# Kernel tuning notes

Hardware: AMD Instinct MI355X
Metric: run time of the kernel (lower is better)

The kernel has to match this reference:

```python
import jax, jax.numpy as jnp
import numpy as np

NUM_HEADS = 8

def _proj(x, W, b):
    # 1x1 conv == channel-wise linear: x [B,Ci,H,W], W [Co,Ci], b [Co]
    return jnp.einsum('oi,bihw->bohw', W, x) + b[None, :, None, None]

def setup_inputs() -> dict:
    key = jax.random.key(0)
    ks = jax.random.split(key, 8)
    B, Cin, Cout, H, W = 4, 256, 256, 48, 48
    s = 1.0 / np.sqrt(Cin).astype(np.float32)
    return {
        'queries': jax.random.normal(ks[0], (B, Cin, H, W), jnp.float32),
        'keys':    jax.random.normal(ks[1], (B, Cin, H, W), jnp.float32),
        'values':  jax.random.normal(ks[2], (B, Cin, H, W), jnp.float32),
        'Wq': jax.random.normal(ks[3], (Cout, Cin), jnp.float32) * s,
        'bq': jnp.zeros((Cout,), jnp.float32),
        'Wk': jax.random.normal(ks[4], (Cout, Cin), jnp.float32) * s,
        'bk': jnp.zeros((Cout,), jnp.float32),
        'Wv': jax.random.normal(ks[5], (Cout, Cin), jnp.float32) * s,
        'bv': jnp.zeros((Cout,), jnp.float32),
        'Wo': jax.random.normal(ks[6], (Cout, Cout), jnp.float32) * s,
        'bo': jnp.zeros((Cout,), jnp.float32),
    }

def reference(queries, keys, values, Wq, bq, Wk, bk, Wv, bv, Wo, bo):
    B, _, H, W = values.shape
    Cout = Wq.shape[0]
    d = Cout // NUM_HEADS
    # project and split heads: [B, heads, d, N]
    q = _proj(queries, Wq, bq).reshape(B, NUM_HEADS, d, H * W)
    k = _proj(keys,    Wk, bk).reshape(B, NUM_HEADS, d, H * W)
    v = _proj(values,  Wv, bv).reshape(B, NUM_HEADS, d, H * W)
    scale = 1.0 / np.sqrt(Cout).astype(np.float32)  # source scales by sqrt(out_channels)
    attn = jax.nn.softmax(jnp.einsum('bhdn,bhdm->bhnm', q, k) * scale, axis=-1)
    out = jnp.einsum('bhdm,bhnm->bhdn', v, attn).reshape(B, Cout, H, W)
    return _proj(out, Wo, bo)
```

## Files before the change

kernel.cpp:

```cpp
#include <hip/hip_runtime.h>
#include <hip/hip_bf16.h>

#define NTOT 2304
#define CIN  256
#define DHEAD 32

typedef float  f32x4  __attribute__((ext_vector_type(4)));
typedef __bf16 bf16x8 __attribute__((ext_vector_type(8)));
typedef unsigned short u16x8 __attribute__((ext_vector_type(8)));

static __device__ __forceinline__ unsigned short f2bf(float f) {
    unsigned int u = __float_as_uint(f);
    u += 0x7fff + ((u >> 16) & 1);
    return (unsigned short)(u >> 16);
}

static __device__ __forceinline__ unsigned int pk2(float a, float b) {
    unsigned int r;
    asm("v_cvt_pk_bf16_f32 %0, %1, %2" : "=v"(r) : "v"(a), "v"(b));
    return r;
}

union U8 { unsigned short s[8]; bf16x8 v; };
union PB { unsigned int u[4]; bf16x8 v; };

__global__ __launch_bounds__(256) void pack_weights_kernel(
    const float* __restrict__ Wq, const float* __restrict__ bq,
    const float* __restrict__ Wk, const float* __restrict__ Wv,
    const float* __restrict__ Wo,
    unsigned short* __restrict__ Wq_b, unsigned short* __restrict__ Wk_b,
    unsigned short* __restrict__ Wv_b, unsigned short* __restrict__ Wo_b,
    float* __restrict__ bq_s)
{
    const float SQ = 1.44269504088896340736f / 16.0f;
    int i = blockIdx.x * 256 + threadIdx.x;
    Wq_b[i] = f2bf(Wq[i] * SQ);
    Wk_b[i] = f2bf(Wk[i]);
    Wv_b[i] = f2bf(Wv[i]);
    Wo_b[i] = f2bf(Wo[i]);
    if (blockIdx.x == 0) bq_s[threadIdx.x] = bq[threadIdx.x] * SQ;
}

__global__ __launch_bounds__(256) void proj_all_kernel(
    const float* __restrict__ qx, const float* __restrict__ kx,
    const float* __restrict__ vx,
    const unsigned short* __restrict__ Wqb, const unsigned short* __restrict__ Wkb,
    const unsigned short* __restrict__ Wvb,
    const float* __restrict__ bqs, const float* __restrict__ bk,
    const float* __restrict__ bv,
    unsigned short* __restrict__ Qa, unsigned short* __restrict__ Ka,
    unsigned short* __restrict__ Vp)
{
    const int which = blockIdx.z >> 2;
    const int b     = blockIdx.z & 3;
    const float* x = (which == 0) ? qx : (which == 1) ? kx : vx;
    const unsigned short* Wb = (which == 0) ? Wqb : (which == 1) ? Wkb : Wvb;
    const float* bias = (which == 0) ? bqs : (which == 1) ? bk : bv;
    unsigned short* out = (which == 0) ? Qa : (which == 1) ? Ka : Vp;

    const int n0  = blockIdx.x * 64;
    const int co0 = blockIdx.y * 64;
    const int t = threadIdx.x;
    const int lane = t & 63, w = t >> 6;
    const int g = lane >> 4, l15 = lane & 15;
    const int n_off  = (w & 1) * 32;
    const int co_off = (w >> 1) * 32;

    f32x4 acc[2][2] = {};
    const float* xb = x + (size_t)b * CIN * NTOT;

    for (int ci0 = 0; ci0 < CIN; ci0 += 32) {
        bf16x8 aF[2], bF[2];
        #pragma unroll
        for (int rn = 0; rn < 2; rn++) {
            const float* xp = xb + (size_t)(ci0 + 8 * g) * NTOT + (n0 + n_off + 16 * rn + l15);
            U8 a;
            #pragma unroll
            for (int j = 0; j < 8; j++) a.s[j] = f2bf(xp[(size_t)j * NTOT]);
            aF[rn] = a.v;
        }
        #pragma unroll
        for (int rc = 0; rc < 2; rc++)
            bF[rc] = *reinterpret_cast<const bf16x8*>(
                Wb + (size_t)(co0 + co_off + 16 * rc + l15) * CIN + ci0 + 8 * g);
        #pragma unroll
        for (int rn = 0; rn < 2; rn++)
            #pragma unroll
            for (int rc = 0; rc < 2; rc++)
                acc[rn][rc] = __builtin_amdgcn_mfma_f32_16x16x32_bf16(aF[rn], bF[rc], acc[rn][rc], 0, 0, 0);
    }

    #pragma unroll
    for (int rn = 0; rn < 2; rn++)
    #pragma unroll
    for (int rc = 0; rc < 2; rc++) {
        int co = co0 + co_off + 16 * rc + l15;
        float bs = bias[co];
        int bh = b * 8 + (co >> 5);
        int dd = co & 31;
        int nb = n0 + n_off + 16 * rn + 4 * g;
        if (which == 2) {
            ushort4 v;
            v.x = f2bf(acc[rn][rc][0] + bs);
            v.y = f2bf(acc[rn][rc][1] + bs);
            v.z = f2bf(acc[rn][rc][2] + bs);
            v.w = f2bf(acc[rn][rc][3] + bs);
            int pos = (nb & ~31) + 8 * ((nb >> 2) & 3) + 4 * ((nb >> 4) & 1);
            *reinterpret_cast<ushort4*>(out + ((size_t)bh * DHEAD + dd) * NTOT + pos) = v;
        } else {
            #pragma unroll
            for (int reg = 0; reg < 4; reg++)
                out[((size_t)bh * NTOT + (nb + reg)) * DHEAD + dd] = f2bf(acc[rn][rc][reg] + bs);
        }
    }
}

__global__ __launch_bounds__(256) void attn_kernel(
    const unsigned short* __restrict__ Qa,
    const unsigned short* __restrict__ Ka,
    const unsigned short* __restrict__ Vp,
    unsigned short* __restrict__ Ot)
{
    __shared__ __align__(16) float olds_a[3][64][17];
    __shared__ __align__(16) float olds_b[3][64][17];
    __shared__ float plsum_a[3][64][3];
    __shared__ float plsum_b[3][64][3];
    __shared__ __align__(16) unsigned short tlds[32][40];
    const int f = blockIdx.x;
    const int c = f & 7;
    const int k = f >> 3;
    const int kq = k / 36;
    const int bh = 4 * c + kq;
    const int qt = k - kq * 36;
    const int b = bh >> 3, h = bh & 7;
    const int t = threadIdx.x;
    const int w = t >> 6, lane = t & 63;
    const int g = lane >> 4, l15 = lane & 15;
    const int n_w = qt * 64;
    const int kw0 = w * 576;

    const unsigned short* Kb = Ka + (size_t)bh * NTOT * DHEAD + l15 * DHEAD + 8 * g;
    const unsigned short* V0 = Vp + ((size_t)bh * DHEAD +      l15) * NTOT + 8 * g;
    const unsigned short* V1 = Vp + ((size_t)bh * DHEAD + 16 + l15) * NTOT + 8 * g;

    bf16x8 qBa[2], qBb[2];
    #pragma unroll
    for (int r = 0; r < 2; r++) {
        qBa[r] = *reinterpret_cast<const bf16x8*>(
            Qa + ((size_t)bh * NTOT + n_w + 16 * r + l15) * DHEAD + 8 * g);
        qBb[r] = *reinterpret_cast<const bf16x8*>(
            Qa + ((size_t)bh * NTOT + n_w + 32 + 16 * r + l15) * DHEAD + 8 * g);
    }

    f32x4 oacc_a[2][2] = {};
    f32x4 oacc_b[2][2] = {};
    float psum_a[2] = {0.f, 0.f};
    float psum_b[2] = {0.f, 0.f};
    const f32x4 z4 = {0.f, 0.f, 0.f, 0.f};

    bf16x8 kA[4], kN[4], vA[4], vN[4];
    #pragma unroll
    for (int mc = 0; mc < 4; mc++) {
        kA[mc] = *reinterpret_cast<const bf16x8*>(Kb + (size_t)(kw0 + 16 * mc) * DHEAD);
        kN[mc] = *reinterpret_cast<const bf16x8*>(Kb + (size_t)(kw0 + 64 + 16 * mc) * DHEAD);
    }
    vA[0] = *reinterpret_cast<const bf16x8*>(V0 + kw0);
    vA[1] = *reinterpret_cast<const bf16x8*>(V0 + kw0 + 32);
    vA[2] = *reinterpret_cast<const bf16x8*>(V1 + kw0);
    vA[3] = *reinterpret_cast<const bf16x8*>(V1 + kw0 + 32);
    vN[0] = *reinterpret_cast<const bf16x8*>(V0 + kw0 + 64);
    vN[1] = *reinterpret_cast<const bf16x8*>(V0 + kw0 + 96);
    vN[2] = *reinterpret_cast<const bf16x8*>(V1 + kw0 + 64);
    vN[3] = *reinterpret_cast<const bf16x8*>(V1 + kw0 + 96);

    for (int it = 0; it < 9; it++) {
        {
            f32x4 s[2][4];
            #pragma unroll
            for (int r = 0; r < 2; r++)
                #pragma unroll
                for (int mc = 0; mc < 4; mc++)
                    s[r][mc] = __builtin_amdgcn_mfma_f32_16x16x32_bf16(kA[mc], qBa[r], z4, 0, 0, 0);

            float p[2][4][4];
            #pragma unroll
            for (int r = 0; r < 2; r++) {
                #pragma unroll
                for (int mc = 0; mc < 4; mc++)
                    #pragma unroll
                    for (int reg = 0; reg < 4; reg++)
                        p[r][mc][reg] = __builtin_amdgcn_exp2f(s[r][mc][reg]);
                float t0 = (p[r][0][0] + p[r][0][1]) + (p[r][0][2] + p[r][0][3]);
                float t1 = (p[r][1][0] + p[r][1][1]) + (p[r][1][2] + p[r][1][3]);
                float t2 = (p[r][2][0] + p[r][2][1]) + (p[r][2][2] + p[r][2][3]);
                float t3 = (p[r][3][0] + p[r][3][1]) + (p[r][3][2] + p[r][3][3]);
                psum_a[r] += (t0 + t1) + (t2 + t3);
            }

            PB pb[2][2];
            #pragma unroll
            for (int r = 0; r < 2; r++)
                #pragma unroll
                for (int hh = 0; hh < 2; hh++) {
                    pb[r][hh].u[0] = pk2(p[r][2*hh][0],   p[r][2*hh][1]);
                    pb[r][hh].u[1] = pk2(p[r][2*hh][2],   p[r][2*hh][3]);
                    pb[r][hh].u[2] = pk2(p[r][2*hh+1][0], p[r][2*hh+1][1]);
                    pb[r][hh].u[3] = pk2(p[r][2*hh+1][2], p[r][2*hh+1][3]);
                }

            #pragma unroll
            for (int r = 0; r < 2; r++) {
                oacc_a[r][0] = __builtin_amdgcn_mfma_f32_16x16x32_bf16(vA[0], pb[r][0].v, oacc_a[r][0], 0, 0, 0);
                oacc_a[r][0] = __builtin_amdgcn_mfma_f32_16x16x32_bf16(vA[1], pb[r][1].v, oacc_a[r][0], 0, 0, 0);
                oacc_a[r][1] = __builtin_amdgcn_mfma_f32_16x16x32_bf16(vA[2], pb[r][0].v, oacc_a[r][1], 0, 0, 0);
                oacc_a[r][1] = __builtin_amdgcn_mfma_f32_16x16x32_bf16(vA[3], pb[r][1].v, oacc_a[r][1], 0, 0, 0);
            }
        }
        {
            f32x4 s[2][4];
            #pragma unroll
            for (int r = 0; r < 2; r++)
                #pragma unroll
                for (int mc = 0; mc < 4; mc++)
                    s[r][mc] = __builtin_amdgcn_mfma_f32_16x16x32_bf16(kA[mc], qBb[r], z4, 0, 0, 0);

            float p[2][4][4];
            #pragma unroll
            for (int r = 0; r < 2; r++) {
                #pragma unroll
                for (int mc = 0; mc < 4; mc++)
                    #pragma unroll
                    for (int reg = 0; reg < 4; reg++)
                        p[r][mc][reg] = __builtin_amdgcn_exp2f(s[r][mc][reg]);
                float t0 = (p[r][0][0] + p[r][0][1]) + (p[r][0][2] + p[r][0][3]);
                float t1 = (p[r][1][0] + p[r][1][1]) + (p[r][1][2] + p[r][1][3]);
                float t2 = (p[r][2][0] + p[r][2][1]) + (p[r][2][2] + p[r][2][3]);
                float t3 = (p[r][3][0] + p[r][3][1]) + (p[r][3][2] + p[r][3][3]);
                psum_b[r] += (t0 + t1) + (t2 + t3);
            }

            PB pb[2][2];
            #pragma unroll
            for (int r = 0; r < 2; r++)
                #pragma unroll
                for (int hh = 0; hh < 2; hh++) {
                    pb[r][hh].u[0] = pk2(p[r][2*hh][0],   p[r][2*hh][1]);
                    pb[r][hh].u[1] = pk2(p[r][2*hh][2],   p[r][2*hh][3]);
                    pb[r][hh].u[2] = pk2(p[r][2*hh+1][0], p[r][2*hh+1][1]);
                    pb[r][hh].u[3] = pk2(p[r][2*hh+1][2], p[r][2*hh+1][3]);
                }

            #pragma unroll
            for (int r = 0; r < 2; r++) {
                oacc_b[r][0] = __builtin_amdgcn_mfma_f32_16x16x32_bf16(vA[0], pb[r][0].v, oacc_b[r][0], 0, 0, 0);
                oacc_b[r][0] = __builtin_amdgcn_mfma_f32_16x16x32_bf16(vA[1], pb[r][1].v, oacc_b[r][0], 0, 0, 0);
                oacc_b[r][1] = __builtin_amdgcn_mfma_f32_16x16x32_bf16(vA[2], pb[r][0].v, oacc_b[r][1], 0, 0, 0);
                oacc_b[r][1] = __builtin_amdgcn_mfma_f32_16x16x32_bf16(vA[3], pb[r][1].v, oacc_b[r][1], 0, 0, 0);
            }
        }

        int m2 = kw0 + (it + 2) * 64;
        if (it >= 7) m2 = kw0;
        #pragma unroll
        for (int mc = 0; mc < 4; mc++) {
            kA[mc] = kN[mc];
            kN[mc] = *reinterpret_cast<const bf16x8*>(Kb + (size_t)(m2 + 16 * mc) * DHEAD);
        }
        vA[0] = vN[0]; vA[1] = vN[1]; vA[2] = vN[2]; vA[3] = vN[3];
        vN[0] = *reinterpret_cast<const bf16x8*>(V0 + m2);
        vN[1] = *reinterpret_cast<const bf16x8*>(V0 + m2 + 32);
        vN[2] = *reinterpret_cast<const bf16x8*>(V1 + m2);
        vN[3] = *reinterpret_cast<const bf16x8*>(V1 + m2 + 32);
    }

    if (w > 0) {
        #pragma unroll
        for (int r = 0; r < 2; r++)
            #pragma unroll
            for (int dc = 0; dc < 2; dc++) {
                *reinterpret_cast<f32x4*>(&olds_a[w - 1][lane][8 * r + 4 * dc]) = oacc_a[r][dc];
                *reinterpret_cast<f32x4*>(&olds_b[w - 1][lane][8 * r + 4 * dc]) = oacc_b[r][dc];
            }
        plsum_a[w - 1][lane][0] = psum_a[0];
        plsum_a[w - 1][lane][1] = psum_a[1];
        plsum_b[w - 1][lane][0] = psum_b[0];
        plsum_b[w - 1][lane][1] = psum_b[1];
    }
    __syncthreads();
    if (w == 0) {
        #pragma unroll
        for (int ww = 0; ww < 3; ww++) {
            #pragma unroll
            for (int r = 0; r < 2; r++)
                #pragma unroll
                for (int dc = 0; dc < 2; dc++)
                    oacc_a[r][dc] += *reinterpret_cast<const f32x4*>(&olds_a[ww][lane][8 * r + 4 * dc]);
            psum_a[0] += plsum_a[ww][lane][0];
            psum_a[1] += plsum_a[ww][lane][1];
        }
        float lra[2];
        #pragma unroll
        for (int r = 0; r < 2; r++) {
            float ps = psum_a[r];
            ps += __shfl_xor(ps, 16);
            ps += __shfl_xor(ps, 32);
            lra[r] = 1.0f / ps;
        }
        #pragma unroll
        for (int r = 0; r < 2; r++)
            #pragma unroll
            for (int dc = 0; dc < 2; dc++) {
                ushort4 v;
                v.x = f2bf(oacc_a[r][dc][0] * lra[r]);
                v.y = f2bf(oacc_a[r][dc][1] * lra[r]);
                v.z = f2bf(oacc_a[r][dc][2] * lra[r]);
                v.w = f2bf(oacc_a[r][dc][3] * lra[r]);
                *reinterpret_cast<ushort4*>(&tlds[16 * r + l15][16 * dc + 4 * g]) = v;
            }
        #pragma unroll
        for (int i = 0; i < 2; i++) {
            int row = 16 * i + (lane >> 2), seg = lane & 3;
            u16x8 val = *reinterpret_cast<const u16x8*>(&tlds[row][seg * 8]);
            *reinterpret_cast<u16x8*>(
                Ot + ((size_t)b * NTOT + n_w + row) * CIN + h * DHEAD + seg * 8) = val;
        }

        #pragma unroll
        for (int ww = 0; ww < 3; ww++) {
            #pragma unroll
            for (int r = 0; r < 2; r++)
                #pragma unroll
                for (int dc = 0; dc < 2; dc++)
                    oacc_b[r][dc] += *reinterpret_cast<const f32x4*>(&olds_b[ww][lane][8 * r + 4 * dc]);
            psum_b[0] += plsum_b[ww][lane][0];
            psum_b[1] += plsum_b[ww][lane][1];
        }
        float lrb[2];
        #pragma unroll
        for (int r = 0; r < 2; r++) {
            float ps = psum_b[r];
            ps += __shfl_xor(ps, 16);
            ps += __shfl_xor(ps, 32);
            lrb[r] = 1.0f / ps;
        }
        #pragma unroll
        for (int r = 0; r < 2; r++)
            #pragma unroll
            for (int dc = 0; dc < 2; dc++) {
                ushort4 v;
                v.x = f2bf(oacc_b[r][dc][0] * lrb[r]);
                v.y = f2bf(oacc_b[r][dc][1] * lrb[r]);
                v.z = f2bf(oacc_b[r][dc][2] * lrb[r]);
                v.w = f2bf(oacc_b[r][dc][3] * lrb[r]);
                *reinterpret_cast<ushort4*>(&tlds[16 * r + l15][16 * dc + 4 * g]) = v;
            }
        #pragma unroll
        for (int i = 0; i < 2; i++) {
            int row = 16 * i + (lane >> 2), seg = lane & 3;
            u16x8 val = *reinterpret_cast<const u16x8*>(&tlds[row][seg * 8]);
            *reinterpret_cast<u16x8*>(
                Ot + ((size_t)b * NTOT + n_w + 32 + row) * CIN + h * DHEAD + seg * 8) = val;
        }
    }
}

__global__ __launch_bounds__(256) void out_proj_kernel(
    const unsigned short* __restrict__ Ot,
    const unsigned short* __restrict__ Wob,
    const float* __restrict__ bo,
    float* __restrict__ out)
{
    const int b   = blockIdx.z;
    const int n0  = blockIdx.x * 64;
    const int co0 = blockIdx.y * 64;
    const int t = threadIdx.x;
    const int lane = t & 63, w = t >> 6;
    const int g = lane >> 4, l15 = lane & 15;
    const int n_off  = (w & 1) * 32;
    const int co_off = (w >> 1) * 32;

    f32x4 acc[2][2] = {};
    for (int ci0 = 0; ci0 < CIN; ci0 += 32) {
        bf16x8 aF[2], bF[2];
        #pragma unroll
        for (int rn = 0; rn < 2; rn++)
            aF[rn] = *reinterpret_cast<const bf16x8*>(
                Ot + ((size_t)b * NTOT + n0 + n_off + 16 * rn + l15) * CIN + ci0 + 8 * g);
        #pragma unroll
        for (int rc = 0; rc < 2; rc++)
            bF[rc] = *reinterpret_cast<const bf16x8*>(
                Wob + (size_t)(co0 + co_off + 16 * rc + l15) * CIN + ci0 + 8 * g);
        #pragma unroll
        for (int rn = 0; rn < 2; rn++)
            #pragma unroll
            for (int rc = 0; rc < 2; rc++)
                acc[rn][rc] = __builtin_amdgcn_mfma_f32_16x16x32_bf16(aF[rn], bF[rc], acc[rn][rc], 0, 0, 0);
    }

    #pragma unroll
    for (int rn = 0; rn < 2; rn++)
    #pragma unroll
    for (int rc = 0; rc < 2; rc++) {
        int co = co0 + co_off + 16 * rc + l15;
        float bias = bo[co];
        int nb = n0 + n_off + 16 * rn + 4 * g;
        float4 v;
        v.x = acc[rn][rc][0] + bias;
        v.y = acc[rn][rc][1] + bias;
        v.z = acc[rn][rc][2] + bias;
        v.w = acc[rn][rc][3] + bias;
        *reinterpret_cast<float4*>(out + ((size_t)b * CIN + co) * NTOT + nb) = v;
    }
}

extern "C" void kernel_launch(void* const* d_in, const int* in_sizes, int n_in,
                              void* d_out, int out_size, void* d_ws, size_t ws_size,
                              hipStream_t stream) {
    const float* qx = (const float*)d_in[0];
    const float* kx = (const float*)d_in[1];
    const float* vx = (const float*)d_in[2];
    const float* Wq = (const float*)d_in[3];
    const float* bq = (const float*)d_in[4];
    const float* Wk = (const float*)d_in[5];
    const float* bk = (const float*)d_in[6];
    const float* Wv = (const float*)d_in[7];
    const float* bv = (const float*)d_in[8];
    const float* Wo = (const float*)d_in[9];
    const float* bo = (const float*)d_in[10];
    float* out = (float*)d_out;

    char* ws = (char*)d_ws;
    unsigned short* Wq_b = (unsigned short*)(ws + 0);
    unsigned short* Wk_b = (unsigned short*)(ws + 131072);
    unsigned short* Wv_b = (unsigned short*)(ws + 262144);
    unsigned short* Wo_b = (unsigned short*)(ws + 393216);
    float*          bq_s = (float*)(ws + 524288);
    unsigned short* Qa   = (unsigned short*)(ws + 525312);
    unsigned short* Ka   = (unsigned short*)(ws + 525312 + 1 * 4718592);
    unsigned short* Vp   = (unsigned short*)(ws + 525312 + 2 * 4718592);
    unsigned short* Ot   = (unsigned short*)(ws + 525312 + 3 * 4718592);

    pack_weights_kernel<<<256, 256, 0, stream>>>(Wq, bq, Wk, Wv, Wo,
                                                 Wq_b, Wk_b, Wv_b, Wo_b, bq_s);
    proj_all_kernel<<<dim3(36, 4, 12), 256, 0, stream>>>(
        qx, kx, vx, Wq_b, Wk_b, Wv_b, bq_s, bk, bv, Qa, Ka, Vp);
    attn_kernel<<<dim3(1152), 256, 0, stream>>>(Qa, Ka, Vp, Ot);
    out_proj_kernel<<<dim3(36, 4, 4), 256, 0, stream>>>(Ot, Wo_b, bo, out);
}
```

Baseline: 94.92 us.

## Compute all output channels per projection block to read activations once

The QKV projection kernel now has each block cover all 256 output channels for its 64 spatial positions. Each wave handles 16 positions across 16 channel tiles, where before it handled a 32x32 sub-tile. The fp32 activations are loaded and converted to bf16 once instead of four times, at the cost of 64 accumulator registers per lane. The grid shrinks by a factor of four to 432 blocks, which may leave the GPU underfilled.

```diff
diff --git a/kernel.cpp b/kernel.cpp
--- a/kernel.cpp
+++ b/kernel.cpp
@@ -58,59 +58,48 @@
     const float* bias = (which == 0) ? bqs : (which == 1) ? bk : bv;
     unsigned short* out = (which == 0) ? Qa : (which == 1) ? Ka : Vp;
 
-    const int n0  = blockIdx.x * 64;
-    const int co0 = blockIdx.y * 64;
+    const int n0 = blockIdx.x * 64;
     const int t = threadIdx.x;
     const int lane = t & 63, w = t >> 6;
     const int g = lane >> 4, l15 = lane & 15;
-    const int n_off  = (w & 1) * 32;
-    const int co_off = (w >> 1) * 32;
-
-    f32x4 acc[2][2] = {};
+    const int nw = n0 + w * 16;
+
+    f32x4 acc[16] = {};
     const float* xb = x + (size_t)b * CIN * NTOT;
 
     for (int ci0 = 0; ci0 < CIN; ci0 += 32) {
-        bf16x8 aF[2], bF[2];
-        #pragma unroll
-        for (int rn = 0; rn < 2; rn++) {
-            const float* xp = xb + (size_t)(ci0 + 8 * g) * NTOT + (n0 + n_off + 16 * rn + l15);
-            U8 a;
-            #pragma unroll
-            for (int j = 0; j < 8; j++) a.s[j] = f2bf(xp[(size_t)j * NTOT]);
-            aF[rn] = a.v;
-        }
-        #pragma unroll
-        for (int rc = 0; rc < 2; rc++)
-            bF[rc] = *reinterpret_cast<const bf16x8*>(
-                Wb + (size_t)(co0 + co_off + 16 * rc + l15) * CIN + ci0 + 8 * g);
-        #pragma unroll
-        for (int rn = 0; rn < 2; rn++)
-            #pragma unroll
-            for (int rc = 0; rc < 2; rc++)
-                acc[rn][rc] = __builtin_amdgcn_mfma_f32_16x16x32_bf16(aF[rn], bF[rc], acc[rn][rc], 0, 0, 0);
+        const float* xp = xb + (size_t)(ci0 + 8 * g) * NTOT + (nw + l15);
+        U8 a;
+        #pragma unroll
+        for (int j = 0; j < 8; j++) a.s[j] = f2bf(xp[(size_t)j * NTOT]);
+        bf16x8 aF = a.v;
+        #pragma unroll
+        for (int rc = 0; rc < 16; rc++) {
+            bf16x8 bF = *reinterpret_cast<const bf16x8*>(
+                Wb + (size_t)(16 * rc + l15) * CIN + ci0 + 8 * g);
+            acc[rc] = __builtin_amdgcn_mfma_f32_16x16x32_bf16(aF, bF, acc[rc], 0, 0, 0);
+        }
     }
 
     #pragma unroll
-    for (int rn = 0; rn < 2; rn++)
-    #pragma unroll
-    for (int rc = 0; rc < 2; rc++) {
-        int co = co0 + co_off + 16 * rc + l15;
+    for (int rc = 0; rc < 16; rc++) {
+        int co = 16 * rc + l15;
         float bs = bias[co];
         int bh = b * 8 + (co >> 5);
         int dd = co & 31;
-        int nb = n0 + n_off + 16 * rn + 4 * g;
+        int nb = nw + 4 * g;
         if (which == 2) {
             ushort4 v;
-            v.x = f2bf(acc[rn][rc][0] + bs);
-            v.y = f2bf(acc[rn][rc][1] + bs);
-            v.z = f2bf(acc[rn][rc][2] + bs);
-            v.w = f2bf(acc[rn][rc][3] + bs);
+            v.x = f2bf(acc[rc][0] + bs);
+            v.y = f2bf(acc[rc][1] + bs);
+            v.z = f2bf(acc[rc][2] + bs);
+            v.w = f2bf(acc[rc][3] + bs);
             int pos = (nb & ~31) + 8 * ((nb >> 2) & 3) + 4 * ((nb >> 4) & 1);
             *reinterpret_cast<ushort4*>(out + ((size_t)bh * DHEAD + dd) * NTOT + pos) = v;
         } else {
             #pragma unroll
             for (int reg = 0; reg < 4; reg++)
-                out[((size_t)bh * NTOT + (nb + reg)) * DHEAD + dd] = f2bf(acc[rn][rc][reg] + bs);
+                out[((size_t)bh * NTOT + (nb + reg)) * DHEAD + dd] = f2bf(acc[rc][reg] + bs);
         }
     }
 }
@@ -442,7 +431,7 @@
 
     pack_weights_kernel<<<256, 256, 0, stream>>>(Wq, bq, Wk, Wv, Wo,
                                                  Wq_b, Wk_b, Wv_b, Wo_b, bq_s);
-    proj_all_kernel<<<dim3(36, 4, 12), 256, 0, stream>>>(
+    proj_all_kernel<<<dim3(36, 1, 12), 256, 0, stream>>>(
         qx, kx, vx, Wq_b, Wk_b, Wv_b, bq_s, bk, bv, Qa, Ka, Vp);
     attn_kernel<<<dim3(1152), 256, 0, stream>>>(Qa, Ka, Vp, Ot);
     out_proj_kernel<<<dim3(36, 4, 4), 256, 0, stream>>>(Ot, Wo_b, bo, out);
```

New measurement: 103.2 us. 8.7% more time.
